# Performance work log

Hardware: AMD Instinct MI355X
Metric: run time of the kernel (lower is better)

The kernel has to match this reference:

```python
import jax, jax.numpy as jnp
import numpy as np

B, T, P = 256, 1024, 32
HOME = 0  # home_idx from init_kwargs


def setup_inputs() -> dict:
    key = jax.random.key(0)
    k1, k2 = jax.random.split(key, 2)
    U = jax.random.normal(k1, (B, T, P), dtype=jnp.float32)
    A = jax.random.uniform(k2, (P, P), dtype=jnp.float32, minval=-0.01, maxval=0.01)
    bias = jnp.zeros((P,), dtype=jnp.float32)
    return {"unary_logits_btp": U, "A": A, "bias": bias}


def reference(unary_logits_btp, A, bias):
    """Constrained Viterbi decode (enforce at least one non-home state).
    State is (purpose p, visited-nonhome flag v in {0,1}). Returns paths (B,T) int32."""
    U = unary_logits_btp + bias  # (B,T,P), bias broadcast as in decode()
    Bn, Tn, Pn = U.shape
    NEG = jnp.finfo(U.dtype).min / 4
    is_home = jnp.arange(Pn) == HOME  # (P,)

    # t=0: v=0 only at home, v=1 only at non-home
    d0 = jnp.where(is_home, U[:, 0], NEG)
    d1 = jnp.where(is_home, NEG, U[:, 0])
    delta0 = jnp.stack([d0, d1], axis=-1)  # (B,P,2)

    def step(delta, U_t):
        # prev{v}[b, q, p] = delta[b, q, v] + A[q, p]
        prev0 = delta[:, :, 0][:, :, None] + A  # (B,P,P)
        prev1 = delta[:, :, 1][:, :, None] + A
        a0 = jnp.argmax(prev0, axis=1).astype(jnp.int32)
        v0 = jnp.max(prev0, axis=1)  # (B,P)
        a1 = jnp.argmax(prev1, axis=1).astype(jnp.int32)
        v1 = jnp.max(prev1, axis=1)
        use1 = v1 > v0  # strict >, matching torch.where(val_from1 > val_from0, ...)
        bval = jnp.where(use1, v1, v0)
        bq = jnp.where(use1, a1, a0)
        bv = use1.astype(jnp.int32)
        # next v=0 reachable only at home (from prev v=0)
        dn0 = jnp.where(is_home, v0 + U_t, NEG)
        # next v=1: home from prev v=1; non-home from best of prev v=0/v=1
        dn1 = jnp.where(is_home, v1, bval) + U_t
        p1 = jnp.where(is_home, a1, bq)
        vv1 = jnp.where(is_home, 1, bv).astype(jnp.int32)
        delta_new = jnp.stack([dn0, dn1], axis=-1)          # (B,P,2)
        psi_p = jnp.stack([a0, p1], axis=-1)                # (B,P,2) best prev purpose
        psi_v = jnp.stack([jnp.zeros_like(vv1), vv1], -1)   # (B,P,2) best prev flag
        return delta_new, (psi_p, psi_v)

    Us = jnp.swapaxes(U, 0, 1)  # (T,B,P)
    delta_T, (psi_p, psi_v) = jax.lax.scan(step, delta0, Us[1:])  # psi_*: (T-1,B,P,2)

    last_p = jnp.argmax(delta_T[:, :, 1], axis=1).astype(jnp.int32)  # (B,)
    b_idx = jnp.arange(Bn)

    def back(carry, psi):
        y, v = carry  # (B,), (B,)
        pp, pv = psi  # (B,P,2)
        py = pp[b_idx, y, v]
        nv = pv[b_idx, y, v]
        return (py, nv), py

    _, ys = jax.lax.scan(back, (last_p, jnp.ones((Bn,), jnp.int32)), (psi_p, psi_v),
                         reverse=True)  # ys: (T-1,B) with ys[t] = y[t]
    paths = jnp.concatenate([jnp.swapaxes(ys, 0, 1), last_p[:, None]], axis=1)  # (B,T)
    return paths
```

## Files before the change

kernel.cpp:

```cpp
#include <hip/hip_runtime.h>

#define T_LEN 1024
#define P_DIM 32
#define HOME_IDX 0
#define NCHUNK 32
#define CHUNK 32


__launch_bounds__(1024, 1)
__global__ void crf_viterbi_kernel(const float* __restrict__ U,
                                   const float* __restrict__ A,
                                   const float* __restrict__ bias,
                                   int* __restrict__ out)
{
    __shared__ __align__(16) float4 sdelta[P_DIM / 4];
    __shared__ unsigned char spsi[(T_LEN - 1) * P_DIM];
    __shared__ unsigned char Mmap[NCHUNK * P_DIM];
    __shared__ unsigned char ent[NCHUNK];
    __shared__ int last_p_sh;

    const int tid = threadIdx.x;
    const int b   = blockIdx.x;
    int* __restrict__ outb = out + (size_t)b * T_LEN;

    if (tid < 64) {
        const int lane = tid;
        const int p    = lane & 31;
        const float NEG = -(3.4028234663852886e38f / 4.0f);

        float Areg[32];
#pragma unroll
        for (int q = 0; q < 32; ++q)
            Areg[q] = A[q * P_DIM + p];
        const float A0p    = Areg[0];
        const float A00    = A[0];
        const float bias_p = bias[p];
        const float bias0  = bias[0];
        const bool  is_home = (p == HOME_IDX);

        const float* __restrict__ Ub = U + (size_t)b * T_LEN * P_DIM;

        const float u00 = Ub[p] + bias_p;
        float delta1  = is_home ? NEG : u00;
        float delta0h = Ub[HOME_IDX] + bias0;

        float L0 = Ub[1 * P_DIM + p];
        float L1 = Ub[2 * P_DIM + p];
        float L2 = Ub[3 * P_DIM + p];
        float L3 = Ub[4 * P_DIM + p];

        float Ut_n = L0 + bias_p;
        float u0_n = __shfl(Ut_n, 0);

        ((float*)sdelta)[p] = delta1;
        float4 R0 = sdelta[0], R1 = sdelta[1], R2 = sdelta[2], R3 = sdelta[3];
        float4 R4 = sdelta[4], R5 = sdelta[5], R6 = sdelta[6], R7 = sdelta[7];

#define STEP(t, Lc, Lr) do {                                                   \
    const float Ut  = Ut_n;                                                    \
    const float u0c = u0_n;                                                    \
    Ut_n = (Lc) + bias_p;                                                      \
    u0_n = __shfl(Ut_n, 0);                                                    \
    { int tn = (t) + 4; if (tn > T_LEN - 1) tn = T_LEN - 1;                    \
      (Lr) = Ub[(size_t)tn * P_DIM + p]; }                                     \
    float c[32];                                                               \
    c[0]=R0.x+Areg[0];  c[1]=R0.y+Areg[1];  c[2]=R0.z+Areg[2];  c[3]=R0.w+Areg[3];   \
    c[4]=R1.x+Areg[4];  c[5]=R1.y+Areg[5];  c[6]=R1.z+Areg[6];  c[7]=R1.w+Areg[7];   \
    c[8]=R2.x+Areg[8];  c[9]=R2.y+Areg[9];  c[10]=R2.z+Areg[10]; c[11]=R2.w+Areg[11];\
    c[12]=R3.x+Areg[12]; c[13]=R3.y+Areg[13]; c[14]=R3.z+Areg[14]; c[15]=R3.w+Areg[15];\
    c[16]=R4.x+Areg[16]; c[17]=R4.y+Areg[17]; c[18]=R4.z+Areg[18]; c[19]=R4.w+Areg[19];\
    c[20]=R5.x+Areg[20]; c[21]=R5.y+Areg[21]; c[22]=R5.z+Areg[22]; c[23]=R5.w+Areg[23];\
    c[24]=R6.x+Areg[24]; c[25]=R6.y+Areg[25]; c[26]=R6.z+Areg[26]; c[27]=R6.w+Areg[27];\
    c[28]=R7.x+Areg[28]; c[29]=R7.y+Areg[29]; c[30]=R7.z+Areg[30]; c[31]=R7.w+Areg[31];\
                 \
    const float g0 = fmaxf(fmaxf(c[0],  c[1]),  c[2]);                         \
    const float g1 = fmaxf(fmaxf(c[3],  c[4]),  c[5]);                         \
    const float g2 = fmaxf(fmaxf(c[6],  c[7]),  c[8]);                         \
    const float g3 = fmaxf(fmaxf(c[9],  c[10]), c[11]);                        \
    const float g4 = fmaxf(fmaxf(c[12], c[13]), c[14]);                        \
    const float g5 = fmaxf(fmaxf(c[15], c[16]), c[17]);                        \
    const float g6 = fmaxf(fmaxf(c[18], c[19]), c[20]);                        \
    const float g7 = fmaxf(fmaxf(c[21], c[22]), c[23]);                        \
    const float g8 = fmaxf(fmaxf(c[24], c[25]), c[26]);                        \
    const float g9 = fmaxf(fmaxf(c[27], c[28]), c[29]);                        \
    const float s0 = fmaxf(fmaxf(g0, g1), g2);                                 \
    const float s1 = fmaxf(fmaxf(g3, g4), g5);                                 \
    const float s2 = fmaxf(fmaxf(g6, g7), g8);                                 \
    const float s3 = fmaxf(fmaxf(g9, c[30]), c[31]);                           \
    const float v1 = fmaxf(fmaxf(s0, s1), fmaxf(s2, s3));                      \
    const float v0 = delta0h + A0p;                                            \
    const bool  use1 = (v1 > v0);                    \
    const bool  cond = use1 || is_home;                                        \
    const float sel  = cond ? v1 : v0;                                         \
    const float dn1  = sel + Ut;                                               \
    delta0h = (delta0h + A00) + u0c;                                           \
      \
    ((float*)sdelta)[p] = dn1;                                                 \
    R0 = sdelta[0]; R1 = sdelta[1]; R2 = sdelta[2]; R3 = sdelta[3];            \
    R4 = sdelta[4]; R5 = sdelta[5]; R6 = sdelta[6]; R7 = sdelta[7];            \
      \
    int ia = 0;                                                                \
    _Pragma("unroll")                                                          \
    for (int j = 31; j >= 0; --j)                                              \
        if (c[j] == v1) ia = j;                                                \
    spsi[(size_t)((t) - 1) * P_DIM + p] = (unsigned char)(cond ? (ia | 32) : 0); \
    delta1 = dn1;                                                              \
} while (0)

        STEP(1, L1, L0);
        STEP(2, L2, L1);
        STEP(3, L3, L2);
        for (int t = 4; t <= T_LEN - 4; t += 4) {
            STEP(t + 0, L0, L3);
            STEP(t + 1, L1, L0);
            STEP(t + 2, L2, L1);
            STEP(t + 3, L3, L2);
        }
#undef STEP

        float mv = delta1;
        int   mi = p;
#pragma unroll
        for (int m = 16; m >= 1; m >>= 1) {
            float ov = __shfl_xor(mv, m);
            int   oi = __shfl_xor(mi, m);
            bool take = (ov > mv) || ((ov == mv) && (oi < mi));
            mv = take ? ov : mv;
            mi = take ? oi : mi;
        }
        if (lane == 0) {
            outb[T_LEN - 1] = mi;
            last_p_sh = mi;
        }
    }

    __syncthreads();

    {
        const int c  = tid >> 5;
        const int pp = tid & 31;
        const int i_hi = min((c + 1) * CHUNK, T_LEN - 1);
        const int i_lo = c * CHUNK;
        int y = pp, v = 1;
        for (int i = i_hi - 1; i >= i_lo; --i) {
            const int bt = spsi[i * P_DIM + y];
            const int py = v ? (bt & 31) : 0;
            const int nv = v ? ((bt >> 5) & 1) : 0;
            y = py; v = nv;
        }
        Mmap[c * P_DIM + pp] = (unsigned char)(y | (v << 5));
    }
    __syncthreads();

    if (tid == 0) {
        int y = last_p_sh, v = 1;
        for (int c = NCHUNK - 1; c >= 0; --c) {
            ent[c] = (unsigned char)(y | (v << 5));
            if (v) {
                const int m = Mmap[c * P_DIM + y];
                y = m & 31;
                v = (m >> 5) & 1;
            } else {
                y = 0; v = 0;
            }
        }
    }
    __syncthreads();

    if (tid < NCHUNK) {
        const int c = tid;
        const int i_hi = min((c + 1) * CHUNK, T_LEN - 1);
        const int i_lo = c * CHUNK;
        const int e = ent[c];
        int y = e & 31;
        int v = (e >> 5) & 1;
        for (int i = i_hi - 1; i >= i_lo; --i) {
            const int bt = spsi[i * P_DIM + y];
            const int py = v ? (bt & 31) : 0;
            const int nv = v ? ((bt >> 5) & 1) : 0;
            outb[i] = py;
            y = py; v = nv;
        }
    }
}

extern "C" void kernel_launch(void* const* d_in, const int* in_sizes, int n_in,
                              void* d_out, int out_size, void* d_ws, size_t ws_size,
                              hipStream_t stream) {
    const float* U    = (const float*)d_in[0];
    const float* A    = (const float*)d_in[1];
    const float* bias = (const float*)d_in[2];
    int* out = (int*)d_out;

    const int B = in_sizes[0] / (T_LEN * P_DIM);
    crf_viterbi_kernel<<<B, 1024, 0, stream>>>(U, A, bias, out);
}
```

Measured before the change: 373.5 us.

## Offload Viterbi argmax backpointer computation from serial wavefront to all block threads

The serial forward recursion now only computes max values and stores each step's delta row into a shared history buffer, in chunks of 192 steps. After each chunk, all 1024 threads recompute the candidate sums from the stored history and run the argmax to write the backpointers in parallel. This takes the 32-way equality scan off the serial critical path. In exchange it adds block-wide barriers per chunk, redundant recomputation of the max, and a larger shared memory footprint.

```diff
diff --git a/kernel.cpp b/kernel.cpp
--- a/kernel.cpp
+++ b/kernel.cpp
@@ -3,6 +3,9 @@
 #define T_LEN 1024
 #define P_DIM 32
 #define HOME_IDX 0
+#define FCH 192
+#define NROW 194
+#define DHOFF (NROW * 32)
 #define NCHUNK 32
 #define CHUNK 32
 
@@ -13,7 +16,7 @@
                                    const float* __restrict__ bias,
                                    int* __restrict__ out)
 {
-    __shared__ __align__(16) float4 sdelta[P_DIM / 4];
+    __shared__ __align__(16) float HB[NROW * 32 + NROW];
     __shared__ unsigned char spsi[(T_LEN - 1) * P_DIM];
     __shared__ unsigned char Mmap[NCHUNK * P_DIM];
     __shared__ unsigned char ent[NCHUNK];
@@ -22,57 +25,54 @@
     const int tid = threadIdx.x;
     const int b   = blockIdx.x;
     int* __restrict__ outb = out + (size_t)b * T_LEN;
+    const float4* __restrict__ HB4 = (const float4*)HB;
+
+    const int  p = tid & 31;
+    const bool is_home = (p == HOME_IDX);
+
+    float Acol[32];
+#pragma unroll
+    for (int q = 0; q < 32; ++q)
+        Acol[q] = A[q * P_DIM + p];
+    const float A00    = A[0];
+    const float bias_p = bias[p];
+
+    float delta1 = 0.f, delta0h = 0.f;
+    float L0 = 0.f, L1 = 0.f, L2 = 0.f, L3 = 0.f, Ut_n = 0.f, u0_n = 0.f;
+    float4 R0, R1, R2, R3, R4, R5, R6, R7;
+    const float* __restrict__ Ub = U + (size_t)b * T_LEN * P_DIM;
 
     if (tid < 64) {
-        const int lane = tid;
-        const int p    = lane & 31;
         const float NEG = -(3.4028234663852886e38f / 4.0f);
-
-        float Areg[32];
-#pragma unroll
-        for (int q = 0; q < 32; ++q)
-            Areg[q] = A[q * P_DIM + p];
-        const float A0p    = Areg[0];
-        const float A00    = A[0];
-        const float bias_p = bias[p];
-        const float bias0  = bias[0];
-        const bool  is_home = (p == HOME_IDX);
-
-        const float* __restrict__ Ub = U + (size_t)b * T_LEN * P_DIM;
-
         const float u00 = Ub[p] + bias_p;
-        float delta1  = is_home ? NEG : u00;
-        float delta0h = Ub[HOME_IDX] + bias0;
-
-        float L0 = Ub[1 * P_DIM + p];
-        float L1 = Ub[2 * P_DIM + p];
-        float L2 = Ub[3 * P_DIM + p];
-        float L3 = Ub[4 * P_DIM + p];
-
-        float Ut_n = L0 + bias_p;
-        float u0_n = __shfl(Ut_n, 0);
-
-        ((float*)sdelta)[p] = delta1;
-        float4 R0 = sdelta[0], R1 = sdelta[1], R2 = sdelta[2], R3 = sdelta[3];
-        float4 R4 = sdelta[4], R5 = sdelta[5], R6 = sdelta[6], R7 = sdelta[7];
-
-#define STEP(t, Lc, Lr) do {                                                   \
+        delta1  = is_home ? NEG : u00;
+        delta0h = Ub[HOME_IDX] + bias[0];
+
+        L0 = Ub[1 * P_DIM + p];
+        L1 = Ub[2 * P_DIM + p];
+        L2 = Ub[3 * P_DIM + p];
+        L3 = Ub[4 * P_DIM + p];
+        Ut_n = L0 + bias_p;
+        u0_n = __shfl(Ut_n, 0);
+
+        const int wa = (tid == 32) ? (DHOFF + 0) : p;
+        HB[wa] = (tid == 32) ? delta0h : delta1;
+        R0 = HB4[0]; R1 = HB4[1]; R2 = HB4[2]; R3 = HB4[3];
+        R4 = HB4[4]; R5 = HB4[5]; R6 = HB4[6]; R7 = HB4[7];
+    }
+
+#define STEP(t, ws, Lc, Lr) do {                                               \
     const float Ut  = Ut_n;                                                    \
     const float u0c = u0_n;                                                    \
-    Ut_n = (Lc) + bias_p;                                                      \
-    u0_n = __shfl(Ut_n, 0);                                                    \
-    { int tn = (t) + 4; if (tn > T_LEN - 1) tn = T_LEN - 1;                    \
-      (Lr) = Ub[(size_t)tn * P_DIM + p]; }                                     \
     float c[32];                                                               \
-    c[0]=R0.x+Areg[0];  c[1]=R0.y+Areg[1];  c[2]=R0.z+Areg[2];  c[3]=R0.w+Areg[3];   \
-    c[4]=R1.x+Areg[4];  c[5]=R1.y+Areg[5];  c[6]=R1.z+Areg[6];  c[7]=R1.w+Areg[7];   \
-    c[8]=R2.x+Areg[8];  c[9]=R2.y+Areg[9];  c[10]=R2.z+Areg[10]; c[11]=R2.w+Areg[11];\
-    c[12]=R3.x+Areg[12]; c[13]=R3.y+Areg[13]; c[14]=R3.z+Areg[14]; c[15]=R3.w+Areg[15];\
-    c[16]=R4.x+Areg[16]; c[17]=R4.y+Areg[17]; c[18]=R4.z+Areg[18]; c[19]=R4.w+Areg[19];\
-    c[20]=R5.x+Areg[20]; c[21]=R5.y+Areg[21]; c[22]=R5.z+Areg[22]; c[23]=R5.w+Areg[23];\
-    c[24]=R6.x+Areg[24]; c[25]=R6.y+Areg[25]; c[26]=R6.z+Areg[26]; c[27]=R6.w+Areg[27];\
-    c[28]=R7.x+Areg[28]; c[29]=R7.y+Areg[29]; c[30]=R7.z+Areg[30]; c[31]=R7.w+Areg[31];\
-                 \
+    c[0]=R0.x+Acol[0];  c[1]=R0.y+Acol[1];  c[2]=R0.z+Acol[2];  c[3]=R0.w+Acol[3];   \
+    c[4]=R1.x+Acol[4];  c[5]=R1.y+Acol[5];  c[6]=R1.z+Acol[6];  c[7]=R1.w+Acol[7];   \
+    c[8]=R2.x+Acol[8];  c[9]=R2.y+Acol[9];  c[10]=R2.z+Acol[10]; c[11]=R2.w+Acol[11];\
+    c[12]=R3.x+Acol[12]; c[13]=R3.y+Acol[13]; c[14]=R3.z+Acol[14]; c[15]=R3.w+Acol[15];\
+    c[16]=R4.x+Acol[16]; c[17]=R4.y+Acol[17]; c[18]=R4.z+Acol[18]; c[19]=R4.w+Acol[19];\
+    c[20]=R5.x+Acol[20]; c[21]=R5.y+Acol[21]; c[22]=R5.z+Acol[22]; c[23]=R5.w+Acol[23];\
+    c[24]=R6.x+Acol[24]; c[25]=R6.y+Acol[25]; c[26]=R6.z+Acol[26]; c[27]=R6.w+Acol[27];\
+    c[28]=R7.x+Acol[28]; c[29]=R7.y+Acol[29]; c[30]=R7.z+Acol[30]; c[31]=R7.w+Acol[31];\
     const float g0 = fmaxf(fmaxf(c[0],  c[1]),  c[2]);                         \
     const float g1 = fmaxf(fmaxf(c[3],  c[4]),  c[5]);                         \
     const float g2 = fmaxf(fmaxf(c[6],  c[7]),  c[8]);                         \
@@ -83,41 +83,104 @@
     const float g7 = fmaxf(fmaxf(c[21], c[22]), c[23]);                        \
     const float g8 = fmaxf(fmaxf(c[24], c[25]), c[26]);                        \
     const float g9 = fmaxf(fmaxf(c[27], c[28]), c[29]);                        \
-    const float s0 = fmaxf(fmaxf(g0, g1), g2);                                 \
-    const float s1 = fmaxf(fmaxf(g3, g4), g5);                                 \
-    const float s2 = fmaxf(fmaxf(g6, g7), g8);                                 \
-    const float s3 = fmaxf(fmaxf(g9, c[30]), c[31]);                           \
-    const float v1 = fmaxf(fmaxf(s0, s1), fmaxf(s2, s3));                      \
-    const float v0 = delta0h + A0p;                                            \
+    const float m0 = fmaxf(fmaxf(g0, g1), g2);                                 \
+    const float m1 = fmaxf(fmaxf(g3, g4), g5);                                 \
+    const float m2 = fmaxf(fmaxf(g6, g7), g8);                                 \
+    const float m3 = fmaxf(fmaxf(g9, c[30]), c[31]);                           \
+    const float v1 = fmaxf(fmaxf(m0, m1), fmaxf(m2, m3));                      \
+    const float v0 = delta0h + Acol[0];                                        \
     const bool  use1 = (v1 > v0);                    \
     const bool  cond = use1 || is_home;                                        \
     const float sel  = cond ? v1 : v0;                                         \
     const float dn1  = sel + Ut;                                               \
     delta0h = (delta0h + A00) + u0c;                                           \
-      \
-    ((float*)sdelta)[p] = dn1;                                                 \
-    R0 = sdelta[0]; R1 = sdelta[1]; R2 = sdelta[2]; R3 = sdelta[3];            \
-    R4 = sdelta[4]; R5 = sdelta[5]; R6 = sdelta[6]; R7 = sdelta[7];            \
-      \
-    int ia = 0;                                                                \
-    _Pragma("unroll")                                                          \
-    for (int j = 31; j >= 0; --j)                                              \
-        if (c[j] == v1) ia = j;                                                \
-    spsi[(size_t)((t) - 1) * P_DIM + p] = (unsigned char)(cond ? (ia | 32) : 0); \
+           \
+    const int wa_ = (tid == 32) ? (DHOFF + (ws)) : ((ws) * 32 + p);            \
+    HB[wa_] = (tid == 32) ? delta0h : dn1;                                     \
+    R0 = HB4[(ws)*8+0]; R1 = HB4[(ws)*8+1]; R2 = HB4[(ws)*8+2]; R3 = HB4[(ws)*8+3]; \
+    R4 = HB4[(ws)*8+4]; R5 = HB4[(ws)*8+5]; R6 = HB4[(ws)*8+6]; R7 = HB4[(ws)*8+7]; \
+                                      \
+    Ut_n = (Lc) + bias_p;                                                      \
+    u0_n = __shfl(Ut_n, 0);                                                    \
+    { int tn = (t) + 4; if (tn > T_LEN - 1) tn = T_LEN - 1;                    \
+      (Lr) = Ub[(size_t)tn * P_DIM + p]; }                                     \
     delta1 = dn1;                                                              \
 } while (0)
 
-        STEP(1, L1, L0);
-        STEP(2, L2, L1);
-        STEP(3, L3, L2);
-        for (int t = 4; t <= T_LEN - 4; t += 4) {
-            STEP(t + 0, L0, L3);
-            STEP(t + 1, L1, L0);
-            STEP(t + 2, L2, L1);
-            STEP(t + 3, L3, L2);
-        }
+    for (int a = 0; a < T_LEN - 1; a += FCH) {
+        const int ns   = (T_LEN - 1 - a < FCH) ? (T_LEN - 1 - a) : FCH;
+        const int kpar = (a / FCH) & 1;
+
+        if (tid < 64) {
+            STEP(a + 1, 1, L1, L0);
+            STEP(a + 2, 2, L2, L1);
+            STEP(a + 3, 3, L3, L2);
+            for (int s = 4; s + 3 <= ns; s += 4) {
+                STEP(a + s + 0, s + 0, L0, L3);
+                STEP(a + s + 1, s + 1, L1, L0);
+                STEP(a + s + 2, s + 2, L2, L1);
+                STEP(a + s + 3, s + 3, L3, L2);
+            }
+            if (ns == FCH)
+                STEP(a + FCH, FCH + kpar, L0, L3);
+        }
+        __syncthreads();
+
+        {
+            const int sg = tid >> 5;
+#pragma unroll
+            for (int pass = 0; pass < FCH / 32; ++pass) {
+                const int s = 1 + sg + 32 * pass;
+                if (s <= ns) {
+                    const int rs = (s == 1)
+                        ? ((a == 0) ? 0 : (FCH + (kpar ^ 1)))
+                        : (s - 1);
+                    const float4 H0 = HB4[rs*8+0], H1 = HB4[rs*8+1];
+                    const float4 H2 = HB4[rs*8+2], H3 = HB4[rs*8+3];
+                    const float4 H4 = HB4[rs*8+4], H5 = HB4[rs*8+5];
+                    const float4 H6 = HB4[rs*8+6], H7 = HB4[rs*8+7];
+                    const float dhp = HB[DHOFF + rs];
+                    float c[32];
+                    c[0]=H0.x+Acol[0];  c[1]=H0.y+Acol[1];  c[2]=H0.z+Acol[2];  c[3]=H0.w+Acol[3];
+                    c[4]=H1.x+Acol[4];  c[5]=H1.y+Acol[5];  c[6]=H1.z+Acol[6];  c[7]=H1.w+Acol[7];
+                    c[8]=H2.x+Acol[8];  c[9]=H2.y+Acol[9];  c[10]=H2.z+Acol[10]; c[11]=H2.w+Acol[11];
+                    c[12]=H3.x+Acol[12]; c[13]=H3.y+Acol[13]; c[14]=H3.z+Acol[14]; c[15]=H3.w+Acol[15];
+                    c[16]=H4.x+Acol[16]; c[17]=H4.y+Acol[17]; c[18]=H4.z+Acol[18]; c[19]=H4.w+Acol[19];
+                    c[20]=H5.x+Acol[20]; c[21]=H5.y+Acol[21]; c[22]=H5.z+Acol[22]; c[23]=H5.w+Acol[23];
+                    c[24]=H6.x+Acol[24]; c[25]=H6.y+Acol[25]; c[26]=H6.z+Acol[26]; c[27]=H6.w+Acol[27];
+                    c[28]=H7.x+Acol[28]; c[29]=H7.y+Acol[29]; c[30]=H7.z+Acol[30]; c[31]=H7.w+Acol[31];
+                    const float g0 = fmaxf(fmaxf(c[0],  c[1]),  c[2]);
+                    const float g1 = fmaxf(fmaxf(c[3],  c[4]),  c[5]);
+                    const float g2 = fmaxf(fmaxf(c[6],  c[7]),  c[8]);
+                    const float g3 = fmaxf(fmaxf(c[9],  c[10]), c[11]);
+                    const float g4 = fmaxf(fmaxf(c[12], c[13]), c[14]);
+                    const float g5 = fmaxf(fmaxf(c[15], c[16]), c[17]);
+                    const float g6 = fmaxf(fmaxf(c[18], c[19]), c[20]);
+                    const float g7 = fmaxf(fmaxf(c[21], c[22]), c[23]);
+                    const float g8 = fmaxf(fmaxf(c[24], c[25]), c[26]);
+                    const float g9 = fmaxf(fmaxf(c[27], c[28]), c[29]);
+                    const float m0 = fmaxf(fmaxf(g0, g1), g2);
+                    const float m1 = fmaxf(fmaxf(g3, g4), g5);
+                    const float m2 = fmaxf(fmaxf(g6, g7), g8);
+                    const float m3 = fmaxf(fmaxf(g9, c[30]), c[31]);
+                    const float v1 = fmaxf(fmaxf(m0, m1), fmaxf(m2, m3));
+                    const float v0 = dhp + Acol[0];
+                    const bool use1 = (v1 > v0);
+                    const bool cond = use1 || is_home;
+                    int ia = 31;
+#pragma unroll
+                    for (int j = 30; j >= 0; --j)
+                        if (c[j] == v1) ia = j;
+                    spsi[(size_t)(a + s - 1) * P_DIM + p] =
+                        (unsigned char)(cond ? (ia | 32) : 0);
+                }
+            }
+        }
+        __syncthreads();
+    }
 #undef STEP
 
+    if (tid < 64) {
         float mv = delta1;
         int   mi = p;
 #pragma unroll
@@ -128,12 +191,11 @@
             mv = take ? ov : mv;
             mi = take ? oi : mi;
         }
-        if (lane == 0) {
+        if (tid == 0) {
             outb[T_LEN - 1] = mi;
             last_p_sh = mi;
         }
     }
-
     __syncthreads();
 
     {
```

New measurement: 325.3 us. -12.9%, faster.
